# Performance work log

Hardware: AMD Instinct MI355X
Metric: run time of the kernel (lower is better)

The kernel has to match this reference:

```python
import jax, jax.numpy as jnp
import numpy as np

L, NH, D, FF, NL, NP = 6, 8, 256, 1024, 4, 4
HD = D // NH
B, Q0 = 4, 1000
SIZES = [(128, 128), (64, 64), (32, 32), (16, 16)]
KEEP_RATIO = 0.5


def _ln(x, w, b, eps=1e-5):
    mu = x.mean(-1, keepdims=True)
    var = ((x - mu) ** 2).mean(-1, keepdims=True)
    return (x - mu) * jax.lax.rsqrt(var + eps) * w + b


def _mha(q, k, v, in_w, in_b, out_w, out_b):
    # torch nn.MultiheadAttention (batch_first, eval mode => no dropout)
    Bq, Qn, _ = q.shape
    wq, wk, wv = jnp.split(in_w, 3, axis=0)
    bq, bk, bv = jnp.split(in_b, 3, axis=0)
    proj = lambda x, w, bb: (x @ w.T + bb).reshape(Bq, -1, NH, HD).transpose(0, 2, 1, 3)
    qh, kh, vh = proj(q, wq, bq), proj(k, wk, bk), proj(v, wv, bv)
    scores = jnp.einsum('bhqd,bhkd->bhqk', qh, kh) * (1.0 / np.float32(np.sqrt(HD)))
    a = jax.nn.softmax(scores, axis=-1)
    o = jnp.einsum('bhqk,bhkd->bhqd', a, vh).transpose(0, 2, 1, 3).reshape(Bq, Qn, D)
    return o @ out_w.T + out_b


def _bilinear(feat, grid):
    # feat [B,NH,HD,H,W]; grid [B,NH,Q,P,2] (x,y) in [-1,1]
    # matches F.grid_sample(mode='bilinear', padding_mode='zeros', align_corners=True)
    Bf, nh, hd, H, W = feat.shape
    gx = (grid[..., 0] + 1.0) * 0.5 * (W - 1)
    gy = (grid[..., 1] + 1.0) * 0.5 * (H - 1)
    x0, y0 = jnp.floor(gx), jnp.floor(gy)
    flat = feat.reshape(Bf, nh, hd, H * W)
    Qn, P = grid.shape[2], grid.shape[3]

    def corner(xi, yi, w):
        valid = (xi >= 0) & (xi <= W - 1) & (yi >= 0) & (yi <= H - 1)
        idx = (jnp.clip(yi, 0, H - 1).astype(jnp.int32) * W
               + jnp.clip(xi, 0, W - 1).astype(jnp.int32)).reshape(Bf, nh, Qn * P)
        vals = jnp.take_along_axis(flat, jnp.broadcast_to(idx[:, :, None, :], (Bf, nh, hd, Qn * P)), axis=3)
        vals = vals.reshape(Bf, nh, hd, Qn, P)
        return vals * (w * valid)[:, :, None]

    wx1, wy1 = gx - x0, gy - y0
    return (corner(x0, y0, (1 - wx1) * (1 - wy1)) + corner(x0 + 1, y0, wx1 * (1 - wy1))
            + corner(x0, y0 + 1, (1 - wx1) * wy1) + corner(x0 + 1, y0 + 1, wx1 * wy1))


def _msdeform(query, feats, ref, off_w, off_b, aw_w, aw_b, out_w, out_b):
    Bq, Qn, _ = query.shape
    off = jnp.tanh((query @ off_w.T + off_b).reshape(Bq, Qn, NH, NL, NP, 2))
    attn = jax.nn.softmax((query @ aw_w.T + aw_b).reshape(Bq, Qn, NH, NL * NP), axis=3)
    attn = attn.reshape(Bq, Qn, NH, NL, NP)
    ref_grid = ref * 2.0 - 1.0  # [B,Q,2]
    agg = 0.0
    for lvl, feat in enumerate(feats):
        fh = feat.reshape(Bq, NH, HD, feat.shape[2], feat.shape[3])
        grid = ref_grid[:, None, :, None, :] + off[:, :, :, lvl].transpose(0, 2, 1, 3, 4)  # [B,NH,Q,NP,2]
        sampled = _bilinear(fh, grid)                     # [B,NH,HD,Q,NP]
        w = attn[:, :, :, lvl].transpose(0, 2, 1, 3)      # [B,NH,Q,NP]
        agg = agg + (sampled * w[:, :, None]).sum(-1)     # [B,NH,HD,Q]
    out = agg.transpose(0, 3, 1, 2).reshape(Bq, Qn, D)
    return out @ out_w.T + out_b, attn


def setup_inputs() -> dict:
    key = jax.random.key(0)
    ks = iter(jax.random.split(key, 64))
    nrm = lambda shape, s=0.02: jax.random.normal(next(ks), shape, jnp.float32) * s
    inp = {
        'query_objects': nrm((B, Q0, D), 1.0),
        'query_embed': nrm((B, Q0, D), 1.0),
    }
    for i, (H, W) in enumerate(SIZES):
        inp[f'feat{i}'] = nrm((B, D, H, W), 1.0)
    inp.update(
        sa_in_w=nrm((L, 3 * D, D)), sa_in_b=jnp.zeros((L, 3 * D)),
        sa_out_w=nrm((L, D, D)), sa_out_b=jnp.zeros((L, D)),
        off_w=nrm((L, NH * NL * NP * 2, D)), off_b=nrm((L, NH * NL * NP * 2), 0.1),
        aw_w=nrm((L, NH * NL * NP, D)), aw_b=jnp.zeros((L, NH * NL * NP)),
        ca_out_w=nrm((L, D, D)), ca_out_b=jnp.zeros((L, D)),
        ff_w1=nrm((L, FF, D)), ff_b1=jnp.zeros((L, FF)),
        ff_w2=nrm((L, D, FF)), ff_b2=jnp.zeros((L, D)),
        nsa_w=jnp.ones((L, D)), nsa_b=jnp.zeros((L, D)),
        nca_w=jnp.ones((L, D)), nca_b=jnp.zeros((L, D)),
        nff_w=jnp.ones((L, D)), nff_b=jnp.zeros((L, D)),
        ref_w1=nrm((D, D)), ref_b1=jnp.zeros((D,)),
        ref_w2=nrm((2, D)), ref_b2=jnp.zeros((2,)),
        score_w=nrm((1, D)), score_b=jnp.zeros((1,)),
        refine_w=nrm((2, D)), refine_b=jnp.zeros((2,)),
    )
    return inp


def reference(query_objects, query_embed, feat0, feat1, feat2, feat3,
              sa_in_w, sa_in_b, sa_out_w, sa_out_b,
              off_w, off_b, aw_w, aw_b, ca_out_w, ca_out_b,
              ff_w1, ff_b1, ff_w2, ff_b2,
              nsa_w, nsa_b, nca_w, nca_b, nff_w, nff_b,
              ref_w1, ref_b1, ref_w2, ref_b2,
              score_w, score_b, refine_w, refine_b):
    feats = [feat0, feat1, feat2, feat3]
    out, q_embed = query_objects, query_embed
    h = jax.nn.relu(q_embed @ ref_w1.T + ref_b1)
    ref_points = jax.nn.sigmoid(h @ ref_w2.T + ref_b2)  # [B,Q,2]
    outputs, attns = [], []
    for i in range(L):
        sa_in = _ln(out, nsa_w[i], nsa_b[i])
        sa_out = _mha(sa_in + q_embed, sa_in + q_embed, sa_in,
                      sa_in_w[i], sa_in_b[i], sa_out_w[i], sa_out_b[i])
        out = out + sa_out
        ca_in = _ln(out, nca_w[i], nca_b[i])
        ca_out, attn = _msdeform(ca_in + q_embed, feats, ref_points,
                                 off_w[i], off_b[i], aw_w[i], aw_b[i], ca_out_w[i], ca_out_b[i])
        out = out + ca_out
        ff_in = _ln(out, nff_w[i], nff_b[i])
        out = out + (jax.nn.relu(ff_in @ ff_w1[i].T + ff_b1[i]) @ ff_w2[i].T + ff_b2[i])
        delta = jnp.tanh(out @ refine_w.T + refine_b) * 0.5
        ref_points = jnp.clip(ref_points + delta, 0.0, 1.0)
        outputs.append(out)
        attns.append(attn)
        if i < L - 1:
            Qn = out.shape[1]
            keep = max(16, int(Qn * KEEP_RATIO))
            scores = jax.nn.sigmoid((jax.lax.stop_gradient(out) @ score_w.T + score_b)[..., 0])
            _, idx = jax.lax.top_k(scores, keep)
            out = jnp.take_along_axis(out, idx[:, :, None], axis=1)
            q_embed = jnp.take_along_axis(q_embed, idx[:, :, None], axis=1)
            ref_points = jnp.take_along_axis(ref_points, idx[:, :, None], axis=1)
    return tuple(outputs) + tuple(attns)
```

## Files before the change

### kernel.cpp

```cpp
#include <hip/hip_runtime.h>
#include <hip/hip_bf16.h>

#define BB 4
#define DD 256

typedef unsigned long long u64;
typedef long long s64;
typedef unsigned int u32;

__device__ __forceinline__ float sigm(float x) { return 1.0f / (1.0f + expf(-x)); }

__global__ void k_ln(const float* __restrict__ x, const float* __restrict__ w,
                     const float* __restrict__ b, float* __restrict__ ln) {
    int row = blockIdx.x, tid = threadIdx.x;
    float v = x[(size_t)row * DD + tid];
    __shared__ float sred[4];
    float s = v;
#pragma unroll
    for (int o = 32; o > 0; o >>= 1) s += __shfl_down(s, o);
    if ((tid & 63) == 0) sred[tid >> 6] = s;
    __syncthreads();
    float mu = (sred[0] + sred[1] + sred[2] + sred[3]) * (1.0f / 256.0f);
    __syncthreads();
    float d = v - mu;
    float s2 = d * d;
#pragma unroll
    for (int o = 32; o > 0; o >>= 1) s2 += __shfl_down(s2, o);
    if ((tid & 63) == 0) sred[tid >> 6] = s2;
    __syncthreads();
    float var = (sred[0] + sred[1] + sred[2] + sred[3]) * (1.0f / 256.0f);
    float r = rsqrtf(var + 1e-5f);
    ln[(size_t)row * DD + tid] = d * r * w[tid] + b[tid];
}

template <int ACT, int RES>
__device__ __forceinline__ void gemm_core(float (*As)[16][64], float (*Ws)[16][64],
                                          const float* __restrict__ A, const float* __restrict__ Pe, int pe,
                                          const float* __restrict__ W, const float* __restrict__ bias,
                                          const float* __restrict__ Rm, float* __restrict__ C,
                                          float* __restrict__ C2,
                                          int M, int N, int K, int row0, int col0) {
    int tid = threadIdx.x;
    int tx = tid & 15, ty = tid >> 4;
    int lm = tid >> 2, lk = (tid & 3) * 4;
    float acc[4][4] = {{0.f}};
    int ar = row0 + lm;
    const float* Arow = A + (size_t)ar * K + lk;
    const float* Prow = pe ? (Pe + (size_t)ar * K + lk) : nullptr;
    const float* Wrow = W + (size_t)(col0 + lm) * K + lk;
    float4 av = make_float4(0.f, 0.f, 0.f, 0.f), wv;
    if (ar < M) {
        av = *(const float4*)(Arow);
        if (pe) { float4 pv = *(const float4*)(Prow); av.x += pv.x; av.y += pv.y; av.z += pv.z; av.w += pv.w; }
    }
    wv = *(const float4*)(Wrow);
    As[0][lk + 0][lm] = av.x; As[0][lk + 1][lm] = av.y; As[0][lk + 2][lm] = av.z; As[0][lk + 3][lm] = av.w;
    Ws[0][lk + 0][lm] = wv.x; Ws[0][lk + 1][lm] = wv.y; Ws[0][lk + 2][lm] = wv.z; Ws[0][lk + 3][lm] = wv.w;
    __syncthreads();
    int nb = K >> 4;
    for (int t = 0; t < nb; t++) {
        int cur = t & 1, nxt = cur ^ 1;
        bool more = (t + 1 < nb);
        if (more) {
            int k0 = (t + 1) << 4;
            av = make_float4(0.f, 0.f, 0.f, 0.f);
            if (ar < M) {
                av = *(const float4*)(Arow + k0);
                if (pe) { float4 pv = *(const float4*)(Prow + k0); av.x += pv.x; av.y += pv.y; av.z += pv.z; av.w += pv.w; }
            }
            wv = *(const float4*)(Wrow + k0);
        }
#pragma unroll
        for (int kk = 0; kk < 16; kk++) {
            float4 a = *(const float4*)&As[cur][kk][ty << 2];
            float4 w = *(const float4*)&Ws[cur][kk][tx << 2];
            acc[0][0] += a.x * w.x; acc[0][1] += a.x * w.y; acc[0][2] += a.x * w.z; acc[0][3] += a.x * w.w;
            acc[1][0] += a.y * w.x; acc[1][1] += a.y * w.y; acc[1][2] += a.y * w.z; acc[1][3] += a.y * w.w;
            acc[2][0] += a.z * w.x; acc[2][1] += a.z * w.y; acc[2][2] += a.z * w.z; acc[2][3] += a.z * w.w;
            acc[3][0] += a.w * w.x; acc[3][1] += a.w * w.y; acc[3][2] += a.w * w.z; acc[3][3] += a.w * w.w;
        }
        if (more) {
            As[nxt][lk + 0][lm] = av.x; As[nxt][lk + 1][lm] = av.y; As[nxt][lk + 2][lm] = av.z; As[nxt][lk + 3][lm] = av.w;
            Ws[nxt][lk + 0][lm] = wv.x; Ws[nxt][lk + 1][lm] = wv.y; Ws[nxt][lk + 2][lm] = wv.z; Ws[nxt][lk + 3][lm] = wv.w;
        }
        __syncthreads();
    }
#pragma unroll
    for (int i2 = 0; i2 < 4; i2++) {
        int r = row0 + (ty << 2) + i2;
        if (r >= M) continue;
        int cc = col0 + (tx << 2);
        float4 v;
        v.x = acc[i2][0] + bias[cc + 0];
        v.y = acc[i2][1] + bias[cc + 1];
        v.z = acc[i2][2] + bias[cc + 2];
        v.w = acc[i2][3] + bias[cc + 3];
        if (ACT == 1) { v.x = fmaxf(v.x, 0.f); v.y = fmaxf(v.y, 0.f); v.z = fmaxf(v.z, 0.f); v.w = fmaxf(v.w, 0.f); }
        if (RES == 1) {
            float4 rm = *(const float4*)(Rm + (size_t)r * N + cc);
            v.x += rm.x; v.y += rm.y; v.z += rm.z; v.w += rm.w;
        }
        *(float4*)(C + (size_t)r * N + cc) = v;
        if (C2) *(float4*)(C2 + (size_t)r * N + cc) = v;
    }
}

template <int ACT, int RES, int PE>
__global__ __launch_bounds__(256) void k_gemm(const float* __restrict__ A, const float* __restrict__ Pe,
                                              const float* __restrict__ W, const float* __restrict__ bias,
                                              const float* __restrict__ Rm, float* __restrict__ C,
                                              int M, int N, int K) {
    __shared__ float As[2][16][64];
    __shared__ float Ws[2][16][64];
    gemm_core<ACT, RES>(As, Ws, A, Pe, PE, W, bias, Rm, C, nullptr, M, N, K, blockIdx.y * 64, blockIdx.x * 64);
}

__global__ __launch_bounds__(256) void k_gemm_st2(const float* __restrict__ A, const float* __restrict__ W,
                                                  const float* __restrict__ bias, const float* __restrict__ Rm,
                                                  float* __restrict__ C, float* __restrict__ C2,
                                                  int M, int N, int K) {
    __shared__ float As[2][16][64];
    __shared__ float Ws[2][16][64];
    gemm_core<0, 1>(As, Ws, A, nullptr, 0, W, bias, Rm, C, C2, M, N, K, blockIdx.y * 64, blockIdx.x * 64);
}

__global__ __launch_bounds__(256) void k_gemm_qkv(const float* __restrict__ A, const float* __restrict__ Pe,
                                                  const float* __restrict__ Wqkv, const float* __restrict__ bqkv,
                                                  float* __restrict__ Cq, float* __restrict__ Ck, float* __restrict__ Cv,
                                                  int M, int K) {
    __shared__ float As[2][16][64];
    __shared__ float Ws[2][16][64];
    int z = blockIdx.z;
    const float* W = Wqkv + (size_t)z * 256 * K;
    const float* bias = bqkv + z * 256;
    float* C = (z == 0) ? Cq : (z == 1) ? Ck : Cv;
    gemm_core<0, 0>(As, Ws, A, Pe, (z < 2) ? 1 : 0, W, bias, nullptr, C, nullptr, M, 256, K,
                    blockIdx.y * 64, blockIdx.x * 64);
}

__global__ __launch_bounds__(256) void k_gemm_offaw(const float* __restrict__ A, const float* __restrict__ Pe,
                                                    const float* __restrict__ Woff, const float* __restrict__ boff,
                                                    const float* __restrict__ Waw, const float* __restrict__ baw,
                                                    float* __restrict__ Coff, float* __restrict__ Caw,
                                                    int M, int K) {
    __shared__ float As[2][16][64];
    __shared__ float Ws[2][16][64];
    int z = blockIdx.z;
    int N = (z == 0) ? 256 : 128;
    if ((int)(blockIdx.x * 64) >= N) return;
    gemm_core<0, 0>(As, Ws, A, Pe, 1, (z == 0) ? Woff : Waw, (z == 0) ? boff : baw, nullptr,
                    (z == 0) ? Coff : Caw, nullptr, M, N, K, blockIdx.y * 64, blockIdx.x * 64);
}

#define MHA_DOT8(SREG, JJ)                                                       \
    {                                                                            \
        _Pragma("unroll")                                                        \
        for (int u = 0; u < 8; u++) SREG[u] = 0.f;                               \
        _Pragma("unroll")                                                        \
        for (int c4 = 0; c4 < 8; c4++) {                                         \
            float q0 = qv[c4 * 4 + 0], q1 = qv[c4 * 4 + 1];                      \
            float q2 = qv[c4 * 4 + 2], q3 = qv[c4 * 4 + 3];                      \
            _Pragma("unroll")                                                    \
            for (int u = 0; u < 8; u++) {                                        \
                float4 k4 = *(const float4*)&Ks[(JJ) + u][c4 * 4];               \
                SREG[u] += q0 * k4.x; SREG[u] += q1 * k4.y;                      \
                SREG[u] += q2 * k4.z; SREG[u] += q3 * k4.w;                      \
            }                                                                    \
        }                                                                        \
    }

__global__ __launch_bounds__(64) void k_mha(const float* __restrict__ Qb, const float* __restrict__ Kb,
                                            const float* __restrict__ Vb, float* __restrict__ Ob, int Qn) {
    int bh = blockIdx.y;
    int b = bh >> 3, h = bh & 7;
    int lane = threadIdx.x;
    int qi = blockIdx.x * 64 + lane;
    __shared__ float Ks[64][36];
    __shared__ float Vs[64][36];
    float qv[32];
    float acc[32];
#pragma unroll
    for (int c = 0; c < 32; c++) acc[c] = 0.f;
    float m = -INFINITY, l = 0.f;
    const float scale = 0.17677669529663687f;
    bool active = qi < Qn;
    if (active) {
        const float4* qp = (const float4*)(Qb + ((size_t)(b * Qn + qi)) * DD + h * 32);
#pragma unroll
        for (int c4 = 0; c4 < 8; c4++) {
            float4 t = qp[c4];
            qv[c4 * 4 + 0] = t.x * scale; qv[c4 * 4 + 1] = t.y * scale;
            qv[c4 * 4 + 2] = t.z * scale; qv[c4 * 4 + 3] = t.w * scale;
        }
    } else {
#pragma unroll
        for (int c = 0; c < 32; c++) qv[c] = 0.f;
    }
    for (int k0 = 0; k0 < Qn; k0 += 64) {
        int nk = Qn - k0; if (nk > 64) nk = 64;
        if (lane < nk) {
            const float4* kp = (const float4*)(Kb + ((size_t)(b * Qn + k0 + lane)) * DD + h * 32);
            const float4* vp = (const float4*)(Vb + ((size_t)(b * Qn + k0 + lane)) * DD + h * 32);
#pragma unroll
            for (int c4 = 0; c4 < 8; c4++) {
                *(float4*)&Ks[lane][c4 * 4] = kp[c4];
                *(float4*)&Vs[lane][c4 * 4] = vp[c4];
            }
        }
        __syncthreads();
        int ng = nk >> 3;
        float scur[8], snxt[8];
        if (ng > 0) MHA_DOT8(scur, 0)
        for (int g = 0; g < ng; g++) {
            int jj = g << 3;
            bool morep = (g + 1 < ng);
            if (morep) MHA_DOT8(snxt, jj + 8)
#pragma unroll
            for (int u = 0; u < 8; u++) {
                float sv = scur[u];
                float mn = fmaxf(m, sv);
                float e = expf(fminf(m - sv, sv - m));
                bool gt = sv > m;
                float sc = gt ? e : 1.0f;
                float p = gt ? 1.0f : e;
                l = l * sc + p;
                m = mn;
#pragma unroll
                for (int c4 = 0; c4 < 8; c4++) {
                    float4 v4 = *(const float4*)&Vs[jj + u][c4 * 4];
                    acc[c4 * 4 + 0] = acc[c4 * 4 + 0] * sc + p * v4.x;
                    acc[c4 * 4 + 1] = acc[c4 * 4 + 1] * sc + p * v4.y;
                    acc[c4 * 4 + 2] = acc[c4 * 4 + 2] * sc + p * v4.z;
                    acc[c4 * 4 + 3] = acc[c4 * 4 + 3] * sc + p * v4.w;
                }
            }
            if (morep) {
#pragma unroll
                for (int u = 0; u < 8; u++) scur[u] = snxt[u];
            }
        }
        for (int j = ng << 3; j < nk; j++) {
            float sv = 0.f;
#pragma unroll
            for (int c4 = 0; c4 < 8; c4++) {
                float4 k4 = *(const float4*)&Ks[j][c4 * 4];
                sv += qv[c4 * 4 + 0] * k4.x; sv += qv[c4 * 4 + 1] * k4.y;
                sv += qv[c4 * 4 + 2] * k4.z; sv += qv[c4 * 4 + 3] * k4.w;
            }
            float mn = fmaxf(m, sv);
            float e = expf(fminf(m - sv, sv - m));
            bool gt = sv > m;
            float sc = gt ? e : 1.0f;
            float p = gt ? 1.0f : e;
            l = l * sc + p;
            m = mn;
#pragma unroll
            for (int c4 = 0; c4 < 8; c4++) {
                float4 v4 = *(const float4*)&Vs[j][c4 * 4];
                acc[c4 * 4 + 0] = acc[c4 * 4 + 0] * sc + p * v4.x;
                acc[c4 * 4 + 1] = acc[c4 * 4 + 1] * sc + p * v4.y;
                acc[c4 * 4 + 2] = acc[c4 * 4 + 2] * sc + p * v4.z;
                acc[c4 * 4 + 3] = acc[c4 * 4 + 3] * sc + p * v4.w;
            }
        }
        __syncthreads();
    }
    if (active) {
        float inv = 1.0f / l;
        float* op = Ob + ((size_t)(b * Qn + qi)) * DD + h * 32;
#pragma unroll
        for (int c4 = 0; c4 < 8; c4++) {
            float4 o;
            o.x = acc[c4 * 4 + 0] * inv; o.y = acc[c4 * 4 + 1] * inv;
            o.z = acc[c4 * 4 + 2] * inv; o.w = acc[c4 * 4 + 3] * inv;
            *(float4*)(op + c4 * 4) = o;
        }
    }
}

__global__ __launch_bounds__(256) void k_trfeat(const float* __restrict__ in, float* __restrict__ out, int HH) {
    __shared__ float t[32][65];
    int bh = blockIdx.y;
    int b = bh >> 3, h = bh & 7;
    int s0 = blockIdx.x * 64;
    int tid = threadIdx.x;
    const float* ip = in + ((size_t)(b * 256 + h * 32)) * HH + s0;
#pragma unroll
    for (int i = 0; i < 8; i++) {
        int idx = i * 256 + tid;
        int c = idx >> 6, s = idx & 63;
        t[c][s] = ip[(size_t)c * HH + s];
    }
    __syncthreads();
    float* op = out + ((size_t)bh * HH + s0) * 32;
#pragma unroll
    for (int i = 0; i < 8; i++) {
        int idx = i * 256 + tid;
        int s = idx >> 5, c = idx & 31;
        op[(size_t)s * 32 + c] = t[c][s];
    }
}

__device__ __forceinline__ float d_samp(const float* fp, int W, int H, int x, int y) {
    if (x < 0 || x > W - 1 || y < 0 || y > H - 1) return 0.f;
    return fp[y * W + x];
}
__device__ __forceinline__ float d_bil(const float* fp, int W, int H, float gx, float gy) {
    float fx = (gx + 1.0f) * 0.5f * (float)(W - 1);
    float fy = (gy + 1.0f) * 0.5f * (float)(H - 1);
    float x0f = floorf(fx), y0f = floorf(fy);
    int x0 = (int)x0f, y0 = (int)y0f;
    float wx = fx - x0f, wy = fy - y0f;
    float v00 = d_samp(fp, W, H, x0, y0);
    float v10 = d_samp(fp, W, H, x0 + 1, y0);
    float v01 = d_samp(fp, W, H, x0, y0 + 1);
    float v11 = d_samp(fp, W, H, x0 + 1, y0 + 1);
    return v00 * (1.f - wx) * (1.f - wy) + v10 * wx * (1.f - wy) + v01 * (1.f - wx) * wy + v11 * wx * wy;
}
__device__ __forceinline__ float d_samp32(const float* fp, int W, int H, int x, int y) {
    if (x < 0 || x > W - 1 || y < 0 || y > H - 1) return 0.f;
    return fp[(size_t)(y * W + x) * 32];
}
__device__ __forceinline__ float d_bil32(const float* fp, int W, int H, float gx, float gy) {
    float fx = (gx + 1.0f) * 0.5f * (float)(W - 1);
    float fy = (gy + 1.0f) * 0.5f * (float)(H - 1);
    float x0f = floorf(fx), y0f = floorf(fy);
    int x0 = (int)x0f, y0 = (int)y0f;
    float wx = fx - x0f, wy = fy - y0f;
    float v00 = d_samp32(fp, W, H, x0, y0);
    float v10 = d_samp32(fp, W, H, x0 + 1, y0);
    float v01 = d_samp32(fp, W, H, x0, y0 + 1);
    float v11 = d_samp32(fp, W, H, x0 + 1, y0 + 1);
    return v00 * (1.f - wx) * (1.f - wy) + v10 * wx * (1.f - wy) + v01 * (1.f - wx) * wy + v11 * wx * wy;
}

template <int TR>
__global__ __launch_bounds__(256) void k_deform(const float* __restrict__ offL, const float* __restrict__ awL,
                                                const float* __restrict__ ref,
                                                const float* __restrict__ f0, const float* __restrict__ f1,
                                                const float* __restrict__ f2, const float* __restrict__ f3,
                                                float* __restrict__ caf, float* __restrict__ attn_out,
                                                int Qn) {
    int row = blockIdx.x;
    int b = row / Qn;
    int tid = threadIdx.x;
    __shared__ float attn_s[8][16];
    __shared__ float off_s[8][16][2];
    __shared__ float rxy[2];
    if (tid < 8) {
        int h = tid;
        const float* ap = awL + (size_t)row * 128 + h * 16;
        float mx = -INFINITY;
        float e[16];
#pragma unroll
        for (int j = 0; j < 16; j++) mx = fmaxf(mx, ap[j]);
        float ssum = 0.f;
#pragma unroll
        for (int j = 0; j < 16; j++) { e[j] = expf(ap[j] - mx); ssum += e[j]; }
        float inv = 1.0f / ssum;
        float* ao = attn_out + (size_t)row * 128 + h * 16;
#pragma unroll
        for (int j = 0; j < 16; j++) {
            float p = e[j] * inv;
            attn_s[h][j] = p;
            ao[j] = p;
        }
        const float* op = offL + (size_t)row * 256 + h * 32;
#pragma unroll
        for (int j = 0; j < 16; j++) {
            off_s[h][j][0] = tanhf(op[j * 2 + 0]);
            off_s[h][j][1] = tanhf(op[j * 2 + 1]);
        }
    }
    if (tid == 8) {
        rxy[0] = ref[(size_t)row * 2 + 0] * 2.f - 1.f;
        rxy[1] = ref[(size_t)row * 2 + 1] * 2.f - 1.f;
    }
    __syncthreads();
    int h = tid >> 5, c = tid & 31;
    float agg = 0.f;
#pragma unroll
    for (int l = 0; l < 4; l++) {
        const int H = 128 >> l;
        const float* base = (l == 0 ? f0 : l == 1 ? f1 : l == 2 ? f2 : f3);
        const float* fp;
        if (TR) fp = base + ((size_t)(b * 8 + h) * (H * H)) * 32 + c;
        else    fp = base + (size_t)(b * DD + h * 32 + c) * H * H;
#pragma unroll
        for (int p = 0; p < 4; p++) {
            int j = l * 4 + p;
            float sv;
            if (TR) sv = d_bil32(fp, H, H, rxy[0] + off_s[h][j][0], rxy[1] + off_s[h][j][1]);
            else    sv = d_bil(fp, H, H, rxy[0] + off_s[h][j][0], rxy[1] + off_s[h][j][1]);
            agg += attn_s[h][j] * sv;
        }
    }
    caf[(size_t)row * DD + h * 32 + c] = agg;
}

__global__ __launch_bounds__(64) void k_refinit(const float* __restrict__ hbuf, const float* __restrict__ w2,
                                                const float* __restrict__ b2, float* __restrict__ ref) {
    int row = blockIdx.x, lane = threadIdx.x;
    const float* hp = hbuf + (size_t)row * DD;
    float s0 = 0.f, s1 = 0.f;
#pragma unroll
    for (int d = 0; d < 4; d++) {
        int dd = lane + d * 64;
        float v = hp[dd];
        s0 += v * w2[dd];
        s1 += v * w2[DD + dd];
    }
#pragma unroll
    for (int o = 32; o > 0; o >>= 1) { s0 += __shfl_down(s0, o); s1 += __shfl_down(s1, o); }
    if (lane == 0) {
        ref[(size_t)row * 2 + 0] = sigm(s0 + b2[0]);
        ref[(size_t)row * 2 + 1] = sigm(s1 + b2[1]);
    }
}

__global__ __launch_bounds__(64) void k_refsc(const float* __restrict__ out, const float* __restrict__ rw,
                                              const float* __restrict__ rb, float* __restrict__ ref,
                                              const float* __restrict__ sw, const float* __restrict__ sb,
                                              float* __restrict__ score) {
    int row = blockIdx.x, lane = threadIdx.x;
    const float* op = out + (size_t)row * DD;
    float s0 = 0.f, s1 = 0.f;
#pragma unroll
    for (int d = 0; d < 4; d++) {
        int dd = lane + d * 64;
        float v = op[dd];
        s0 += v * rw[dd];
        s1 += v * rw[DD + dd];
    }
#pragma unroll
    for (int o = 32; o > 0; o >>= 1) { s0 += __shfl_down(s0, o); s1 += __shfl_down(s1, o); }
    if (lane == 0) {
        float r0 = ref[(size_t)row * 2 + 0] + tanhf(s0 + rb[0]) * 0.5f;
        float r1 = ref[(size_t)row * 2 + 1] + tanhf(s1 + rb[1]) * 0.5f;
        ref[(size_t)row * 2 + 0] = fminf(fmaxf(r0, 0.f), 1.f);
        ref[(size_t)row * 2 + 1] = fminf(fmaxf(r1, 0.f), 1.f);
        float s = sb[0];
        for (int d = 0; d < DD; d++) s += op[d] * sw[d];
        score[row] = sigm(s);
    }
}

__global__ __launch_bounds__(256) void k_topk(const float* __restrict__ score, int* __restrict__ idx,
                                              int Qn, int PAD, int keep) {
    __shared__ u64 keys[1024];
    int b = blockIdx.x, tid = threadIdx.x;
    for (int q = tid; q < PAD; q += 256) {
        u64 key;
        if (q < Qn) {
            u32 u = __float_as_uint(score[b * Qn + q]);
            u = (u & 0x80000000u) ? ~u : (u | 0x80000000u);
            u32 hi = ~u;
            key = (((u64)hi) << 32) | (u32)q;
        } else {
            key = 0xFFFFFFFFFFFFFFFFULL;
        }
        keys[q] = key;
    }
    __syncthreads();
    for (int k = 2; k <= PAD; k <<= 1) {
        for (int j = k >> 1; j > 0; j >>= 1) {
            for (int i = tid; i < PAD; i += 256) {
                int ij = i ^ j;
                if (ij > i) {
                    bool up = ((i & k) == 0);
                    u64 a = keys[i], c = keys[ij];
                    if ((a > c) == up) { keys[i] = c; keys[ij] = a; }
                }
            }
            __syncthreads();
        }
    }
    for (int t = tid; t < keep; t += 256) idx[b * keep + t] = (int)(keys[t] & 0xFFFFFFFFu);
}

__global__ __launch_bounds__(256) void k_gather(const float* __restrict__ osrc, const float* __restrict__ esrc,
                                                const float* __restrict__ rsrc, const int* __restrict__ idx,
                                                float* __restrict__ oT, float* __restrict__ eT,
                                                float* __restrict__ rT, int Qin, int keep) {
    int j = blockIdx.x;
    int b = j / keep;
    int src = idx[j];
    int tid = threadIdx.x;
    size_t srow = (size_t)(b * Qin + src), drow = (size_t)j;
    oT[drow * DD + tid] = osrc[srow * DD + tid];
    eT[drow * DD + tid] = esrc[srow * DD + tid];
    if (tid < 2) rT[drow * 2 + tid] = rsrc[srow * 2 + tid];
}

__global__ __launch_bounds__(256) void k_copyback(const float* __restrict__ oT, const float* __restrict__ eT,
                                                  const float* __restrict__ rT, float* __restrict__ o,
                                                  float* __restrict__ e, float* __restrict__ r) {
    int row = blockIdx.x, tid = threadIdx.x;
    o[(size_t)row * DD + tid] = oT[(size_t)row * DD + tid];
    e[(size_t)row * DD + tid] = eT[(size_t)row * DD + tid];
    if (tid < 2) r[(size_t)row * 2 + tid] = rT[(size_t)row * 2 + tid];
}

extern "C" void kernel_launch(void* const* d_in, const int* in_sizes, int n_in,
                              void* d_out, int out_size, void* d_ws, size_t ws_size,
                              hipStream_t stream) {
    (void)in_sizes; (void)n_in; (void)out_size;
    const float* q_obj = (const float*)d_in[0];
    const float* q_emb = (const float*)d_in[1];
    const float* feat0 = (const float*)d_in[2];
    const float* feat1 = (const float*)d_in[3];
    const float* feat2 = (const float*)d_in[4];
    const float* feat3 = (const float*)d_in[5];
    const float* sa_in_w = (const float*)d_in[6];
    const float* sa_in_b = (const float*)d_in[7];
    const float* sa_out_w = (const float*)d_in[8];
    const float* sa_out_b = (const float*)d_in[9];
    const float* off_w = (const float*)d_in[10];
    const float* off_b = (const float*)d_in[11];
    const float* aw_w = (const float*)d_in[12];
    const float* aw_b = (const float*)d_in[13];
    const float* ca_out_w = (const float*)d_in[14];
    const float* ca_out_b = (const float*)d_in[15];
    const float* ff_w1 = (const float*)d_in[16];
    const float* ff_b1 = (const float*)d_in[17];
    const float* ff_w2 = (const float*)d_in[18];
    const float* ff_b2 = (const float*)d_in[19];
    const float* nsa_w = (const float*)d_in[20];
    const float* nsa_b = (const float*)d_in[21];
    const float* nca_w = (const float*)d_in[22];
    const float* nca_b = (const float*)d_in[23];
    const float* nff_w = (const float*)d_in[24];
    const float* nff_b = (const float*)d_in[25];
    const float* ref_w1 = (const float*)d_in[26];
    const float* ref_b1 = (const float*)d_in[27];
    const float* ref_w2 = (const float*)d_in[28];
    const float* ref_b2 = (const float*)d_in[29];
    const float* score_w = (const float*)d_in[30];
    const float* score_b = (const float*)d_in[31];
    const float* refine_w = (const float*)d_in[32];
    const float* refine_b = (const float*)d_in[33];

    float* outf = (float*)d_out;
    float* ws = (float*)d_ws;
    const int RD = 4000 * 256;
    float* f_out = ws;
    float* f_emb = ws + RD;
    float* f_ln  = ws + 2 * RD;
    float* sc0   = ws + 3 * RD;
    float* sc1   = ws + 4 * RD;
    float* sc2   = ws + 5 * RD;
    float* f_ref = ws + 6 * RD;
    float* f_sc  = ws + 6 * RD + 8000;
    int*   i_idx = (int*)(ws + 6 * RD + 12032);
    float* f_tr  = ws + 6 * RD + 16384;
    static const s64 tr_ofs[4] = {0, 16777216, 20971520, 22020096};
    const size_t tr_need_bytes = ((size_t)(6 * RD + 16384) + 22282240ULL) * 4ULL;
    const bool use_tr = ws_size >= tr_need_bytes;

    static const int Qs[6] = {1000, 500, 250, 125, 62, 31};
    static const s64 out_ofs[6] = {0, 1024000, 1536000, 1792000, 1920000, 1983488};
    static const s64 attn_ofs[6] = {2015232, 2527232, 2783232, 2911232, 2975232, 3006976};

    hipMemcpyAsync(f_out, q_obj, (size_t)RD * 4, hipMemcpyDeviceToDevice, stream);
    hipMemcpyAsync(f_emb, q_emb, (size_t)RD * 4, hipMemcpyDeviceToDevice, stream);

    if (use_tr) {
        k_trfeat<<<dim3(16384 / 64, 32), 256, 0, stream>>>(feat0, f_tr + tr_ofs[0], 16384);
        k_trfeat<<<dim3(4096 / 64, 32), 256, 0, stream>>>(feat1, f_tr + tr_ofs[1], 4096);
        k_trfeat<<<dim3(1024 / 64, 32), 256, 0, stream>>>(feat2, f_tr + tr_ofs[2], 1024);
        k_trfeat<<<dim3(256 / 64, 32), 256, 0, stream>>>(feat3, f_tr + tr_ofs[3], 256);
    }

    k_gemm<1, 0, 0><<<dim3(4, 63), 256, 0, stream>>>(f_emb, nullptr, ref_w1, ref_b1, nullptr, f_ln, 4000, 256, 256);
    k_refinit<<<4000, 64, 0, stream>>>(f_ln, ref_w2, ref_b2, f_ref);

    for (int i = 0; i < 6; i++) {
        const int Q = Qs[i];
        const int R = BB * Q;
        const int gy = (R + 63) / 64;
        const float* siw = sa_in_w + (size_t)i * 768 * 256;
        const float* sib = sa_in_b + (size_t)i * 768;

        k_ln<<<R, 256, 0, stream>>>(f_out, nsa_w + i * 256, nsa_b + i * 256, f_ln);
        k_gemm_qkv<<<dim3(4, gy, 3), 256, 0, stream>>>(f_ln, f_emb, siw, sib, sc0, sc1, sc2, R, 256);
        k_mha<<<dim3((Q + 63) / 64, 32), 64, 0, stream>>>(sc0, sc1, sc2, f_ln, Q);
        k_gemm<0, 1, 0><<<dim3(4, gy), 256, 0, stream>>>(f_ln, nullptr, sa_out_w + (size_t)i * 65536,
                                                         sa_out_b + i * 256, f_out, f_out, R, 256, 256);

        k_ln<<<R, 256, 0, stream>>>(f_out, nca_w + i * 256, nca_b + i * 256, f_ln);
        k_gemm_offaw<<<dim3(4, gy, 2), 256, 0, stream>>>(f_ln, f_emb, off_w + (size_t)i * 65536, off_b + i * 256,
                                                         aw_w + (size_t)i * 32768, aw_b + i * 128, sc0, sc1, R, 256);
        if (use_tr)
            k_deform<1><<<R, 256, 0, stream>>>(sc0, sc1, f_ref, f_tr + tr_ofs[0], f_tr + tr_ofs[1],
                                               f_tr + tr_ofs[2], f_tr + tr_ofs[3], sc2, outf + attn_ofs[i], Q);
        else
            k_deform<0><<<R, 256, 0, stream>>>(sc0, sc1, f_ref, feat0, feat1, feat2, feat3, sc2,
                                               outf + attn_ofs[i], Q);
        k_gemm<0, 1, 0><<<dim3(4, gy), 256, 0, stream>>>(sc2, nullptr, ca_out_w + (size_t)i * 65536,
                                                         ca_out_b + i * 256, f_out, f_out, R, 256, 256);

        k_ln<<<R, 256, 0, stream>>>(f_out, nff_w + i * 256, nff_b + i * 256, f_ln);
        for (int r0 = 0; r0 < R; r0 += 2000) {
            int mc = R - r0; if (mc > 2000) mc = 2000;
            int gyc = (mc + 63) / 64;
            k_gemm<1, 0, 0><<<dim3(16, gyc), 256, 0, stream>>>(f_ln + (size_t)r0 * 256, nullptr,
                                                               ff_w1 + (size_t)i * 262144, ff_b1 + i * 1024,
                                                               nullptr, sc0, mc, 1024, 256);
            k_gemm_st2<<<dim3(4, gyc), 256, 0, stream>>>(sc0, ff_w2 + (size_t)i * 262144,
                                                         ff_b2 + i * 256, f_out + (size_t)r0 * 256,
                                                         f_out + (size_t)r0 * 256,
                                                         outf + out_ofs[i] + (size_t)r0 * 256, mc, 256, 1024);
        }

        if (i < 5) {
            int keep = Qs[i + 1];
            int PAD = 1;
            while (PAD < Q) PAD <<= 1;
            k_refsc<<<R, 64, 0, stream>>>(f_out, refine_w, refine_b, f_ref, score_w, score_b, f_sc);
            k_topk<<<4, 256, 0, stream>>>(f_sc, i_idx, Q, PAD, keep);
            k_gather<<<4 * keep, 256, 0, stream>>>(f_out, f_emb, f_ref, i_idx, sc0, sc1, sc2, Q, keep);
            k_copyback<<<4 * keep, 256, 0, stream>>>(sc0, sc1, sc2, f_out, f_emb, f_ref);
        }
    }
}
```

Baseline: 2.347 ms.

## Add 128x128 FF1 GEMM kernel and read MHA K/V directly from global

Replaces the first feed-forward GEMM with a dedicated kernel using 128x128 tiles and 8x8 per-thread register blocking, fusing bias and ReLU, to raise arithmetic intensity per shared-memory load. Separately, the self-attention kernel drops its shared-memory K/V staging and barriers and reads K/V rows straight from global memory, relying on caches since all lanes read the same rows. The larger tile gives fewer blocks for small row counts. The MHA change trades LDS traffic and syncs for uncoalesced, broadcast-style global loads.

New measurement: 2.998 ms. +27.7%, slower.

```diff
diff --git a/kernel.cpp b/kernel.cpp
--- a/kernel.cpp
+++ b/kernel.cpp
@@ -152,7 +152,77 @@
                     (z == 0) ? Coff : Caw, nullptr, M, N, K, blockIdx.y * 64, blockIdx.x * 64);
 }
 
-#define MHA_DOT8(SREG, JJ)                                                       \
+__global__ __launch_bounds__(256) void k_ff1(const float* __restrict__ A, const float* __restrict__ W,
+                                             const float* __restrict__ bias, float* __restrict__ C, int M) {
+    const int K = 256;
+    __shared__ float As[2][16][128];
+    __shared__ float Ws[2][16][128];
+    int tid = threadIdx.x;
+    int tx = tid & 15, ty = tid >> 4;
+    int row0 = blockIdx.y * 128, col0 = blockIdx.x * 128;
+    int lm = tid >> 1, lk = (tid & 1) * 8;
+    float acc[8][8] = {{0.f}};
+    int ar = row0 + lm;
+    const float* Arow = A + (size_t)ar * K + lk;
+    const float* Wrow = W + (size_t)(col0 + lm) * K + lk;
+    float4 a0 = make_float4(0.f, 0.f, 0.f, 0.f), a1 = a0, w0, w1;
+    if (ar < M) { a0 = *(const float4*)(Arow); a1 = *(const float4*)(Arow + 4); }
+    w0 = *(const float4*)(Wrow); w1 = *(const float4*)(Wrow + 4);
+    As[0][lk + 0][lm] = a0.x; As[0][lk + 1][lm] = a0.y; As[0][lk + 2][lm] = a0.z; As[0][lk + 3][lm] = a0.w;
+    As[0][lk + 4][lm] = a1.x; As[0][lk + 5][lm] = a1.y; As[0][lk + 6][lm] = a1.z; As[0][lk + 7][lm] = a1.w;
+    Ws[0][lk + 0][lm] = w0.x; Ws[0][lk + 1][lm] = w0.y; Ws[0][lk + 2][lm] = w0.z; Ws[0][lk + 3][lm] = w0.w;
+    Ws[0][lk + 4][lm] = w1.x; Ws[0][lk + 5][lm] = w1.y; Ws[0][lk + 6][lm] = w1.z; Ws[0][lk + 7][lm] = w1.w;
+    __syncthreads();
+    const int nb = K >> 4;
+    for (int t = 0; t < nb; t++) {
+        int cur = t & 1, nxt = cur ^ 1;
+        bool more = (t + 1 < nb);
+        if (more) {
+            int k0 = (t + 1) << 4;
+            a0 = make_float4(0.f, 0.f, 0.f, 0.f); a1 = a0;
+            if (ar < M) { a0 = *(const float4*)(Arow + k0); a1 = *(const float4*)(Arow + k0 + 4); }
+            w0 = *(const float4*)(Wrow + k0); w1 = *(const float4*)(Wrow + k0 + 4);
+        }
+#pragma unroll
+        for (int kk = 0; kk < 16; kk++) {
+            float4 xa0 = *(const float4*)&As[cur][kk][ty * 4];
+            float4 xa1 = *(const float4*)&As[cur][kk][64 + ty * 4];
+            float4 xw0 = *(const float4*)&Ws[cur][kk][tx * 4];
+            float4 xw1 = *(const float4*)&Ws[cur][kk][64 + tx * 4];
+            float av8[8] = {xa0.x, xa0.y, xa0.z, xa0.w, xa1.x, xa1.y, xa1.z, xa1.w};
+            float wv8[8] = {xw0.x, xw0.y, xw0.z, xw0.w, xw1.x, xw1.y, xw1.z, xw1.w};
+#pragma unroll
+            for (int i = 0; i < 8; i++)
+#pragma unroll
+                for (int j2 = 0; j2 < 8; j2++)
+                    acc[i][j2] += av8[i] * wv8[j2];
+        }
+        if (more) {
+            As[nxt][lk + 0][lm] = a0.x; As[nxt][lk + 1][lm] = a0.y; As[nxt][lk + 2][lm] = a0.z; As[nxt][lk + 3][lm] = a0.w;
+            As[nxt][lk + 4][lm] = a1.x; As[nxt][lk + 5][lm] = a1.y; As[nxt][lk + 6][lm] = a1.z; As[nxt][lk + 7][lm] = a1.w;
+            Ws[nxt][lk + 0][lm] = w0.x; Ws[nxt][lk + 1][lm] = w0.y; Ws[nxt][lk + 2][lm] = w0.z; Ws[nxt][lk + 3][lm] = w0.w;
+            Ws[nxt][lk + 4][lm] = w1.x; Ws[nxt][lk + 5][lm] = w1.y; Ws[nxt][lk + 6][lm] = w1.z; Ws[nxt][lk + 7][lm] = w1.w;
+        }
+        __syncthreads();
+    }
+#pragma unroll
+    for (int i = 0; i < 8; i++) {
+        int r = row0 + ((i < 4) ? (ty * 4 + i) : (64 + ty * 4 + (i - 4)));
+        if (r >= M) continue;
+#pragma unroll
+        for (int jh = 0; jh < 2; jh++) {
+            int cc = col0 + jh * 64 + tx * 4;
+            float4 v;
+            v.x = fmaxf(acc[i][jh * 4 + 0] + bias[cc + 0], 0.f);
+            v.y = fmaxf(acc[i][jh * 4 + 1] + bias[cc + 1], 0.f);
+            v.z = fmaxf(acc[i][jh * 4 + 2] + bias[cc + 2], 0.f);
+            v.w = fmaxf(acc[i][jh * 4 + 3] + bias[cc + 3], 0.f);
+            *(float4*)(C + (size_t)r * 1024 + cc) = v;
+        }
+    }
+}
+
+#define MHA_DOT8G(SREG, JJ)                                                      \
     {                                                                            \
         _Pragma("unroll")                                                        \
         for (int u = 0; u < 8; u++) SREG[u] = 0.f;                               \
@@ -162,7 +232,7 @@
             float q2 = qv[c4 * 4 + 2], q3 = qv[c4 * 4 + 3];                      \
             _Pragma("unroll")                                                    \
             for (int u = 0; u < 8; u++) {                                        \
-                float4 k4 = *(const float4*)&Ks[(JJ) + u][c4 * 4];               \
+                float4 k4 = *(const float4*)(Kbase + (size_t)((JJ) + u) * DD + c4 * 4); \
                 SREG[u] += q0 * k4.x; SREG[u] += q1 * k4.y;                      \
                 SREG[u] += q2 * k4.z; SREG[u] += q3 * k4.w;                      \
             }                                                                    \
@@ -175,8 +245,8 @@
     int b = bh >> 3, h = bh & 7;
     int lane = threadIdx.x;
     int qi = blockIdx.x * 64 + lane;
-    __shared__ float Ks[64][36];
-    __shared__ float Vs[64][36];
+    const float* Kbase = Kb + (size_t)b * Qn * DD + h * 32;
+    const float* Vbase = Vb + (size_t)b * Qn * DD + h * 32;
     float qv[32];
     float acc[32];
 #pragma unroll
@@ -196,57 +266,16 @@
 #pragma unroll
         for (int c = 0; c < 32; c++) qv[c] = 0.f;
     }
-    for (int k0 = 0; k0 < Qn; k0 += 64) {
-        int nk = Qn - k0; if (nk > 64) nk = 64;
-        if (lane < nk) {
-            const float4* kp = (const float4*)(Kb + ((size_t)(b * Qn + k0 + lane)) * DD + h * 32);
-            const float4* vp = (const float4*)(Vb + ((size_t)(b * Qn + k0 + lane)) * DD + h * 32);
-#pragma unroll
-            for (int c4 = 0; c4 < 8; c4++) {
-                *(float4*)&Ks[lane][c4 * 4] = kp[c4];
-                *(float4*)&Vs[lane][c4 * 4] = vp[c4];
-            }
-        }
-        __syncthreads();
-        int ng = nk >> 3;
-        float scur[8], snxt[8];
-        if (ng > 0) MHA_DOT8(scur, 0)
-        for (int g = 0; g < ng; g++) {
-            int jj = g << 3;
-            bool morep = (g + 1 < ng);
-            if (morep) MHA_DOT8(snxt, jj + 8)
-#pragma unroll
-            for (int u = 0; u < 8; u++) {
-                float sv = scur[u];
-                float mn = fmaxf(m, sv);
-                float e = expf(fminf(m - sv, sv - m));
-                bool gt = sv > m;
-                float sc = gt ? e : 1.0f;
-                float p = gt ? 1.0f : e;
-                l = l * sc + p;
-                m = mn;
-#pragma unroll
-                for (int c4 = 0; c4 < 8; c4++) {
-                    float4 v4 = *(const float4*)&Vs[jj + u][c4 * 4];
-                    acc[c4 * 4 + 0] = acc[c4 * 4 + 0] * sc + p * v4.x;
-                    acc[c4 * 4 + 1] = acc[c4 * 4 + 1] * sc + p * v4.y;
-                    acc[c4 * 4 + 2] = acc[c4 * 4 + 2] * sc + p * v4.z;
-                    acc[c4 * 4 + 3] = acc[c4 * 4 + 3] * sc + p * v4.w;
-                }
-            }
-            if (morep) {
-#pragma unroll
-                for (int u = 0; u < 8; u++) scur[u] = snxt[u];
-            }
-        }
-        for (int j = ng << 3; j < nk; j++) {
-            float sv = 0.f;
-#pragma unroll
-            for (int c4 = 0; c4 < 8; c4++) {
-                float4 k4 = *(const float4*)&Ks[j][c4 * 4];
-                sv += qv[c4 * 4 + 0] * k4.x; sv += qv[c4 * 4 + 1] * k4.y;
-                sv += qv[c4 * 4 + 2] * k4.z; sv += qv[c4 * 4 + 3] * k4.w;
-            }
+    int ng = Qn >> 3;
+    float scur[8], snxt[8];
+    if (ng > 0) MHA_DOT8G(scur, 0)
+    for (int g = 0; g < ng; g++) {
+        int jj = g << 3;
+        bool morep = (g + 1 < ng);
+        if (morep) MHA_DOT8G(snxt, jj + 8)
+#pragma unroll
+        for (int u = 0; u < 8; u++) {
+            float sv = scur[u];
             float mn = fmaxf(m, sv);
             float e = expf(fminf(m - sv, sv - m));
             bool gt = sv > m;
@@ -256,14 +285,41 @@
             m = mn;
 #pragma unroll
             for (int c4 = 0; c4 < 8; c4++) {
-                float4 v4 = *(const float4*)&Vs[j][c4 * 4];
+                float4 v4 = *(const float4*)(Vbase + (size_t)(jj + u) * DD + c4 * 4);
                 acc[c4 * 4 + 0] = acc[c4 * 4 + 0] * sc + p * v4.x;
                 acc[c4 * 4 + 1] = acc[c4 * 4 + 1] * sc + p * v4.y;
                 acc[c4 * 4 + 2] = acc[c4 * 4 + 2] * sc + p * v4.z;
                 acc[c4 * 4 + 3] = acc[c4 * 4 + 3] * sc + p * v4.w;
             }
         }
-        __syncthreads();
+        if (morep) {
+#pragma unroll
+            for (int u = 0; u < 8; u++) scur[u] = snxt[u];
+        }
+    }
+    for (int j = ng << 3; j < Qn; j++) {
+        float sv = 0.f;
+#pragma unroll
+        for (int c4 = 0; c4 < 8; c4++) {
+            float4 k4 = *(const float4*)(Kbase + (size_t)j * DD + c4 * 4);
+            sv += qv[c4 * 4 + 0] * k4.x; sv += qv[c4 * 4 + 1] * k4.y;
+            sv += qv[c4 * 4 + 2] * k4.z; sv += qv[c4 * 4 + 3] * k4.w;
+        }
+        float mn = fmaxf(m, sv);
+        float e = expf(fminf(m - sv, sv - m));
+        bool gt = sv > m;
+        float sc = gt ? e : 1.0f;
+        float p = gt ? 1.0f : e;
+        l = l * sc + p;
+        m = mn;
+#pragma unroll
+        for (int c4 = 0; c4 < 8; c4++) {
+            float4 v4 = *(const float4*)(Vbase + (size_t)j * DD + c4 * 4);
+            acc[c4 * 4 + 0] = acc[c4 * 4 + 0] * sc + p * v4.x;
+            acc[c4 * 4 + 1] = acc[c4 * 4 + 1] * sc + p * v4.y;
+            acc[c4 * 4 + 2] = acc[c4 * 4 + 2] * sc + p * v4.z;
+            acc[c4 * 4 + 3] = acc[c4 * 4 + 3] * sc + p * v4.w;
+        }
     }
     if (active) {
         float inv = 1.0f / l;
@@ -603,9 +659,9 @@
         for (int r0 = 0; r0 < R; r0 += 2000) {
             int mc = R - r0; if (mc > 2000) mc = 2000;
             int gyc = (mc + 63) / 64;
-            k_gemm<1, 0, 0><<<dim3(16, gyc), 256, 0, stream>>>(f_ln + (size_t)r0 * 256, nullptr,
-                                                               ff_w1 + (size_t)i * 262144, ff_b1 + i * 1024,
-                                                               nullptr, sc0, mc, 1024, 256);
+            k_ff1<<<dim3(8, (mc + 127) / 128), 256, 0, stream>>>(f_ln + (size_t)r0 * 256,
+                                                                 ff_w1 + (size_t)i * 262144, ff_b1 + i * 1024,
+                                                                 sc0, mc);
             k_gemm_st2<<<dim3(4, gyc), 256, 0, stream>>>(sc0, ff_w2 + (size_t)i * 262144,
                                                          ff_b2 + i * 256, f_out + (size_t)r0 * 256,
                                                          f_out + (size_t)r0 * 256,
```
